# Performance work log

Hardware: AMD Instinct MI355X
Metric: run time of the kernel (lower is better)

## Reference

```python
import jax, jax.numpy as jnp
import numpy as np

N, E, F = 50000, 400000, 128
H0, C0 = 1, 128   # layer 0: heads=1, out=128 (concat=False -> mean over heads)
H1, C1 = 4, 64    # layer 1: heads=4, out=64
EPS_BN = 1e-5
NEG_SLOPE = 0.2


def setup_inputs() -> dict:
    key = jax.random.key(0)
    ks = jax.random.split(key, 12)

    def w(k, shape, fan_in):
        return jax.random.normal(k, shape, jnp.float32) / np.float32(np.sqrt(fan_in))

    return {
        "emb": jax.random.normal(ks[0], (N, F), jnp.float32),
        "edge_weight": jax.random.uniform(ks[1], (E,), jnp.float32),
        # GATv2Conv layer 0 params (lin_l, lin_r, lin_edge, att, out bias)
        "Wl0": w(ks[2], (F, H0 * C0), F), "bl0": jnp.zeros((H0 * C0,), jnp.float32),
        "Wr0": w(ks[3], (F, H0 * C0), F), "br0": jnp.zeros((H0 * C0,), jnp.float32),
        "We0": w(ks[4], (1, H0 * C0), 1), "att0": w(ks[5], (H0, C0), C0),
        "b0": jnp.zeros((C0,), jnp.float32),
        "g0": jnp.ones((C0,), jnp.float32), "be0": jnp.zeros((C0,), jnp.float32),
        # GATv2Conv layer 1 params
        "Wl1": w(ks[6], (C0, H1 * C1), C0), "bl1": jnp.zeros((H1 * C1,), jnp.float32),
        "Wr1": w(ks[7], (C0, H1 * C1), C0), "br1": jnp.zeros((H1 * C1,), jnp.float32),
        "We1": w(ks[8], (1, H1 * C1), 1), "att1": w(ks[9], (H1, C1), C1),
        "b1": jnp.zeros((C1,), jnp.float32),
        "g1": jnp.ones((C1,), jnp.float32), "be1": jnp.zeros((C1,), jnp.float32),
        "edge_index": jax.random.randint(ks[10], (2, E), 0, N, jnp.int32),
    }


def gatv2(x, src, dst, ea, Wl, bl, Wr, br, We, att, b, H, C):
    """PyG GATv2Conv, edge_dim=1, concat=False (mean over heads), eval dropout."""
    n = x.shape[0]
    xl = (x @ Wl + bl).reshape(n, H, C)
    xr = (x @ Wr + br).reshape(n, H, C)
    ef = (ea[:, None] @ We).reshape(-1, H, C)           # [Et,H,C] edge embedding
    m = jax.nn.leaky_relu(xl[src] + xr[dst] + ef, NEG_SLOPE)  # [Et,H,C]
    alpha = jnp.einsum('ehc,hc->eh', m, att)            # attention logits
    amax = jax.ops.segment_max(alpha, dst, num_segments=n)
    ex = jnp.exp(alpha - amax[dst])
    den = jax.ops.segment_sum(ex, dst, num_segments=n)
    a = ex / (den[dst] + 1e-16)                          # segment softmax (PyG eps)
    out = jax.ops.segment_sum(a[:, :, None] * xl[src], dst, num_segments=n)
    return out.mean(axis=1) + b                          # concat=False -> head mean


def batchnorm(x, g, be):
    mu = x.mean(0)
    v = x.var(0)  # biased variance, as torch BN uses for normalization
    return g * (x - mu) * jax.lax.rsqrt(v + EPS_BN) + be


def _forward(emb, edge_weight, Wl0, bl0, Wr0, br0, We0, att0, b0, g0, be0,
             Wl1, bl1, Wr1, br1, We1, att1, b1, g1, be1, edge_index):
    loop = jnp.arange(N, dtype=edge_index.dtype)
    src = jnp.concatenate([edge_index[0], loop])
    dst = jnp.concatenate([edge_index[1], loop])
    # add_self_loops with fill_value='mean' for edge_attr
    ea = jnp.concatenate([edge_weight, jnp.full((N,), edge_weight.mean(), edge_weight.dtype)])
    # NOTE: zip(layer_stack, batchnorm_stack) truncates -> only first 2 of 3 GAT
    # layers execute, each followed by BN + ELU (+ identity dropout, p=0).
    h = gatv2(emb, src, dst, ea, Wl0, bl0, Wr0, br0, We0, att0, b0, H0, C0)
    h = jax.nn.elu(batchnorm(h, g0, be0))
    h = gatv2(h, src, dst, ea, Wl1, bl1, Wr1, br1, We1, att1, b1, H1, C1)
    h = jax.nn.elu(batchnorm(h, g1, be1))
    return h


def reference(emb, edge_weight, Wl0, bl0, Wr0, br0, We0, att0, b0, g0, be0,
              Wl1, bl1, Wr1, br1, We1, att1, b1, g1, be1, edge_index):
    return _forward(emb, edge_weight, Wl0, bl0, Wr0, br0, We0, att0, b0, g0, be0,
                    Wl1, bl1, Wr1, br1, We1, att1, b1, g1, be1, edge_index)
```

## Files before the change

### kernel.cpp

```cpp
#include <hip/hip_runtime.h>
#include <cstdint>
#include <cstddef>
#include <type_traits>

using f32x4 = __attribute__((ext_vector_type(4))) float;
using s16x8 = __attribute__((ext_vector_type(8))) short;

__device__ __forceinline__ ushort f2bf(float x) {
    uint32_t u = __builtin_bit_cast(uint32_t, x);
    u += 0x7fffu + ((u >> 16) & 1u);
    return (ushort)(u >> 16);
}
__device__ __forceinline__ float bflo(uint32_t u) { return __builtin_bit_cast(float, u << 16); }
__device__ __forceinline__ float bfhi(uint32_t u) { return __builtin_bit_cast(float, u & 0xffff0000u); }

__device__ __forceinline__ void dec8(uint4 g, float* x) {
    x[0] = bflo(g.x); x[1] = bfhi(g.x); x[2] = bflo(g.y); x[3] = bfhi(g.y);
    x[4] = bflo(g.z); x[5] = bfhi(g.z); x[6] = bflo(g.w); x[7] = bfhi(g.w);
}

#define GLOAD_LDS16(g, l)                                                                  \
    __builtin_amdgcn_global_load_lds((const __attribute__((address_space(1))) void*)(g),  \
                                     (__attribute__((address_space(3))) void*)(l), 16, 0, 0)

__global__ __launch_bounds__(256) void degree_ew_wt(const int* __restrict__ ei,
                                                    const float* __restrict__ ew,
                                                    int* __restrict__ deg,
                                                    float* __restrict__ partials,
                                                    int E, int N, int NBE,
                                                    const float* __restrict__ Wl0,
                                                    const float* __restrict__ Wr0,
                                                    ushort* __restrict__ WT0,
                                                    const float* __restrict__ Wl1,
                                                    const float* __restrict__ Wr1,
                                                    ushort* __restrict__ WT1) {
    __shared__ float red[256];
    int bid = blockIdx.x;
    int t = threadIdx.x;
    if (bid < NBE) {
        int e = bid * 256 + t;
        float s = (e < E) ? ew[e] : 0.f;
        red[t] = s; __syncthreads();
        for (int o = 128; o; o >>= 1) { if (t < o) red[t] += red[t + o]; __syncthreads(); }
        if (t == 0) partials[bid] = red[0];
        if (e < E + N) {
            int d = (e < E) ? ei[E + e] : (e - E);
            atomicAdd(&deg[d], 1);
        }
        return;
    }
    int j = (bid - NBE) * 256 + t;
    if (j < 128 * 256) {
        int k = j >> 8, c = j & 255;
        float v = (c < 128) ? Wl0[k * 128 + c] : Wr0[k * 128 + (c - 128)];
        WT0[(size_t)c * 128 + k] = f2bf(v);
        return;
    }
    j -= 128 * 256;
    if (j < 128 * 512) {
        int k = j >> 9, c = j & 511;
        float v = (c < 256) ? Wl1[k * 256 + c] : Wr1[k * 256 + (c - 256)];
        WT1[(size_t)c * 128 + k] = f2bf(v);
    }
}

__global__ void scan_partial(const int* __restrict__ deg, int n, int* __restrict__ bsum) {
    __shared__ int lds[256];
    int t = threadIdx.x;
    int base = blockIdx.x * 1024 + t * 4;
    int s = 0;
#pragma unroll
    for (int j = 0; j < 4; ++j) if (base + j < n) s += deg[base + j];
    lds[t] = s; __syncthreads();
    for (int o = 128; o; o >>= 1) { if (t < o) lds[t] += lds[t + o]; __syncthreads(); }
    if (t == 0) bsum[blockIdx.x] = lds[0];
}

__global__ void scan_block(const int* __restrict__ bsum, int nb, int* __restrict__ boff,
                           int* __restrict__ row_start, int n, int total,
                           const float* __restrict__ partials, int nbp, int E,
                           float* __restrict__ stats) {
    __shared__ int lds[256];
    __shared__ float fred[256];
    int t = threadIdx.x;
    int v = (t < nb) ? bsum[t] : 0;
    lds[t] = v; __syncthreads();
    for (int o = 1; o < 256; o <<= 1) {
        int y = (t >= o) ? lds[t - o] : 0;
        __syncthreads();
        lds[t] += y;
        __syncthreads();
    }
    if (t < nb) boff[t] = lds[t] - v;
    if (t == 0) row_start[n] = total;
    stats[t] = 0.f; stats[256 + t] = 0.f;
    float fs = 0.f;
    for (int j = t; j < nbp; j += 256) fs += partials[j];
    fred[t] = fs; __syncthreads();
    for (int o = 128; o; o >>= 1) { if (t < o) fred[t] += fred[t + o]; __syncthreads(); }
    if (t == 0) stats[0] = fred[0] / (float)E;
}

__global__ void scan_final(const int* __restrict__ deg, int n, const int* __restrict__ boff,
                           int* __restrict__ row_start, int* __restrict__ cursor) {
    __shared__ int lds[256];
    int t = threadIdx.x;
    int base = blockIdx.x * 1024 + t * 4;
    int d[4], loc[4], s = 0;
#pragma unroll
    for (int j = 0; j < 4; ++j) d[j] = (base + j < n) ? deg[base + j] : 0;
#pragma unroll
    for (int j = 0; j < 4; ++j) { loc[j] = s; s += d[j]; }
    lds[t] = s; __syncthreads();
    for (int o = 1; o < 256; o <<= 1) {
        int y = (t >= o) ? lds[t - o] : 0;
        __syncthreads();
        lds[t] += y;
        __syncthreads();
    }
    int texcl = lds[t] - s + boff[blockIdx.x];
#pragma unroll
    for (int j = 0; j < 4; ++j)
        if (base + j < n) { row_start[base + j] = texcl + loc[j]; cursor[base + j] = 0; }
}

__global__ void scatter_kernel(const int* __restrict__ ei, const float* __restrict__ ew,
                               const float* __restrict__ ew_mean, const int* __restrict__ row_start,
                               int* __restrict__ cursor, int2* __restrict__ csr,
                               int E, int N) {
    int e = blockIdx.x * blockDim.x + threadIdx.x;
    if (e >= E + N) return;
    int s, d; float w;
    if (e < E) { s = ei[e]; d = ei[E + e]; w = ew[e]; }
    else       { s = d = e - E;            w = ew_mean[0]; }
    int pos = row_start[d] + atomicAdd(&cursor[d], 1);
    csr[pos] = make_int2(s, __builtin_bit_cast(int, w));
}

template <int MODE>
__global__ __launch_bounds__(512) void mfma_linear3(const void* __restrict__ Xv,
                                                    const ushort* __restrict__ WT,
                                                    const float* __restrict__ bnsums,
                                                    const float* __restrict__ gamma,
                                                    const float* __restrict__ beta,
                                                    const float* __restrict__ bl,
                                                    const float* __restrict__ br,
                                                    ushort* __restrict__ xl,
                                                    ushort* __restrict__ xr,
                                                    int n, int HALF) {
    constexpr int LW = (MODE == 1) ? 2 : 1;
    __shared__ ushort sB[128 * 128];
    __shared__ ushort sA[128 * 128];
    const int tid = threadIdx.x;
    const int c0 = blockIdx.x * 128;
    const int ntiles = (n + 127) >> 7;

    {
        const ushort* src = WT + (size_t)c0 * 128;
#pragma unroll
        for (int it = 0; it < 4; ++it) {
            int f = tid + it * 512;
            int row = f >> 4, ch = f & 15;
            const ushort* g = src + (size_t)row * 128 + ((ch ^ (row & 7)) << 3);
            ushort* lp = sB + (((size_t)it * 512 + (tid & ~63)) << 3);
            GLOAD_LDS16(g, lp);
        }
    }

    const int myc = (tid & 15) * 8;
    const int row0 = tid >> 4;
    const int swc = (tid & 15) ^ (row0 & 7);
    float Af[8], Bf[8];
    if constexpr (MODE == 2) {
        float invn = 1.f / (float)n;
#pragma unroll
        for (int j = 0; j < 8; ++j) {
            float mu = bnsums[myc + j] * invn;
            float var = bnsums[128 + myc + j] * invn - mu * mu;
            float rs = rsqrtf(var + 1e-5f);
            Af[j] = gamma[myc + j] * rs;
            Bf[j] = beta[myc + j] - mu * Af[j];
        }
    }

    uint4 rA[4][LW];
    auto loadA = [&](int rt) {
        int r0 = rt << 7;
#pragma unroll
        for (int it = 0; it < 4; ++it) {
            int gr = r0 + row0 + it * 32; gr = gr < n ? gr : n - 1;
            if constexpr (MODE == 1) {
                const float* src = (const float*)Xv + (size_t)gr * 128 + myc;
                rA[it][0] = *(const uint4*)src;
                rA[it][1] = *(const uint4*)(src + 4);
            } else {
                rA[it][0] = *(const uint4*)((const ushort*)Xv + (size_t)gr * 128 + myc);
            }
        }
    };
    auto writeA = [&]() {
#pragma unroll
        for (int it = 0; it < 4; ++it) {
            uint4 o;
            if constexpr (MODE == 0) {
                o = rA[it][0];
            } else if constexpr (MODE == 1) {
                float x[8] = {
                    __builtin_bit_cast(float, rA[it][0].x), __builtin_bit_cast(float, rA[it][0].y),
                    __builtin_bit_cast(float, rA[it][0].z), __builtin_bit_cast(float, rA[it][0].w),
                    __builtin_bit_cast(float, rA[it][1].x), __builtin_bit_cast(float, rA[it][1].y),
                    __builtin_bit_cast(float, rA[it][1].z), __builtin_bit_cast(float, rA[it][1].w)};
                ushort h[8];
#pragma unroll
                for (int j = 0; j < 8; ++j) h[j] = f2bf(x[j]);
                o.x = h[0] | ((uint32_t)h[1] << 16); o.y = h[2] | ((uint32_t)h[3] << 16);
                o.z = h[4] | ((uint32_t)h[5] << 16); o.w = h[6] | ((uint32_t)h[7] << 16);
            } else {
                float x[8]; dec8(rA[it][0], x);
                ushort h[8];
#pragma unroll
                for (int j = 0; j < 8; ++j) {
                    float v = fmaf(x[j], Af[j], Bf[j]);
                    v = v > 0.f ? v : __expf(v) - 1.f;
                    h[j] = f2bf(v);
                }
                o.x = h[0] | ((uint32_t)h[1] << 16); o.y = h[2] | ((uint32_t)h[3] << 16);
                o.z = h[4] | ((uint32_t)h[5] << 16); o.w = h[6] | ((uint32_t)h[7] << 16);
            }
            *(uint4*)&sA[(row0 + it * 32) * 128 + swc * 8] = o;
        }
    };

    const int w = tid >> 6, l = tid & 63, lr = l & 15, lg = l >> 4;
    const bool left = c0 < HALF;
    const float* bias = left ? bl : br;
    ushort* dst = left ? xl : xr;
    const int cb = left ? c0 : c0 - HALF;
    float bv[8];
#pragma unroll
    for (int tn = 0; tn < 8; ++tn) bv[tn] = bias[cb + tn * 16 + lr];
    const int arow = w * 16 + lr;

    int rt = blockIdx.y;
    if (rt >= ntiles) return;
    loadA(rt);
    writeA();
    __syncthreads();

    while (true) {
        int nx = rt + gridDim.y;
        if (nx < ntiles) loadA(nx);

        f32x4 acc[8] = {};
#pragma unroll
        for (int kk = 0; kk < 4; ++kk) {
            int ach = (kk * 4 + lg) ^ (arow & 7);
            s16x8 a = *(const s16x8*)&sA[arow * 128 + (ach << 3)];
#pragma unroll
            for (int tn = 0; tn < 8; ++tn) {
                int brow = tn * 16 + lr;
                int bch = (kk * 4 + lg) ^ (brow & 7);
                s16x8 b = *(const s16x8*)&sB[brow * 128 + (bch << 3)];
                acc[tn] = __builtin_amdgcn_mfma_f32_16x16x32_bf16(a, b, acc[tn], 0, 0, 0);
            }
        }
        int rbase = (rt << 7) + w * 16 + lg * 4;
#pragma unroll
        for (int tn = 0; tn < 8; ++tn) {
            int colh = cb + tn * 16 + lr;
#pragma unroll
            for (int r = 0; r < 4; ++r) {
                int row = rbase + r;
                if (row < n) dst[(size_t)row * HALF + colh] = f2bf(acc[tn][r] + bv[tn]);
            }
        }
        if (nx >= ntiles) break;
        __syncthreads();
        writeA();
        __syncthreads();
        rt = nx;
    }
}

template <int H, int C, int LPN>
__global__ __launch_bounds__(256, 6) void gat_agg(const ushort* __restrict__ xl,
                                                  const ushort* __restrict__ xr,
                                                  const int* __restrict__ row_start,
                                                  const int2* __restrict__ csr,
                                                  const float* __restrict__ We,
                                                  const float* __restrict__ att,
                                                  const float* __restrict__ bias,
                                                  ushort* __restrict__ out, int n) {
    constexpr int HC = H * C;
    constexpr int VPL = HC / LPN;
    constexpr int REDW = LPN / H;
    constexpr int NPW = 64 / LPN;
    static_assert(VPL == 8, "");

    const int wid = threadIdx.x >> 6;
    const int lane = threadIdx.x & 63;
    const int sl = lane & (LPN - 1);
    const int sub = lane / LPN;
    const int v = (blockIdx.x * 4 + wid) * NPW + sub;
    const bool valid = v < n;
    const int vv = valid ? v : n - 1;

    const int base = sl * VPL;
    const int e0 = row_start[vv];
    const int e1 = row_start[vv + 1];
    const ushort* xlb = xl + base;

    auto LD = [&](int ee, uint4& g, float& w) {
        ee = ee < e1 - 1 ? ee : e1 - 1;
        int2 sw = csr[ee];
        w = __builtin_bit_cast(float, sw.y);
        g = *(const uint4*)&xlb[(size_t)sw.x * HC];
    };

    uint4 gF; float wF;
    LD(e0, gF, wF);
    uint4 gA, gB; float wA, wB;
    LD(e0 + 1, gA, wA);
    LD(e0 + 2, gB, wB);

    float xrv[8], wE[8], attv[8];
    dec8(*(const uint4*)&xr[(size_t)vv * HC + base], xrv);
#pragma unroll
    for (int j = 0; j < 8; j += 4) {
        float4 a = *(const float4*)&We[base + j];
        wE[j] = a.x; wE[j + 1] = a.y; wE[j + 2] = a.z; wE[j + 3] = a.w;
        float4 b = *(const float4*)&att[base + j];
        attv[j] = b.x; attv[j + 1] = b.y; attv[j + 2] = b.z; attv[j + 3] = b.w;
    }

    float m, den, acc[8];
    {
        float xf[8];
        dec8(gF, xf);
        float t1 = 0.f, t2 = 0.f;
#pragma unroll
        for (int j = 0; j < 8; ++j) {
            float u = xf[j] + fmaf(wF, wE[j], xrv[j]);
            t1 = fmaf(u, attv[j], t1);
            t2 = fmaf(__builtin_fabsf(u), attv[j], t2);
        }
        float p = fmaf(0.6f, t1, 0.4f * t2);
#pragma unroll
        for (int o = REDW >> 1; o; o >>= 1) p += __shfl_xor(p, o, 64);
        m = p; den = 1.f;
#pragma unroll
        for (int j = 0; j < 8; ++j) acc[j] = xf[j];
    }

    int e = e0 + 1;
    while (e + 1 < e1) {
        uint4 g0 = gA, g1 = gB; float w0 = wA, w1 = wB;
        LD(e + 2, gA, wA);
        LD(e + 3, gB, wB);
        float xf0[8], xf1[8];
        dec8(g0, xf0); dec8(g1, xf1);
        float t10 = 0.f, t20 = 0.f, t11 = 0.f, t21 = 0.f;
#pragma unroll
        for (int j = 0; j < 8; ++j) {
            float u0 = xf0[j] + fmaf(w0, wE[j], xrv[j]);
            float u1 = xf1[j] + fmaf(w1, wE[j], xrv[j]);
            t10 = fmaf(u0, attv[j], t10);
            t20 = fmaf(__builtin_fabsf(u0), attv[j], t20);
            t11 = fmaf(u1, attv[j], t11);
            t21 = fmaf(__builtin_fabsf(u1), attv[j], t21);
        }
        float p0 = fmaf(0.6f, t10, 0.4f * t20);
        float p1 = fmaf(0.6f, t11, 0.4f * t21);
#pragma unroll
        for (int o = REDW >> 1; o; o >>= 1) {
            p0 += __shfl_xor(p0, o, 64);
            p1 += __shfl_xor(p1, o, 64);
        }
        float pm = fmaxf(p0, p1);
        if (__builtin_expect(pm - m > 8.f, 0)) {
            float r = __expf(m - pm);
            den *= r;
#pragma unroll
            for (int j = 0; j < 8; ++j) acc[j] *= r;
            m = pm;
        }
        float pe0 = __expf(p0 - m);
        float pe1 = __expf(p1 - m);
        den += pe0 + pe1;
#pragma unroll
        for (int j = 0; j < 8; ++j)
            acc[j] = fmaf(pe1, xf1[j], fmaf(pe0, xf0[j], acc[j]));
        e += 2;
    }
    if (e < e1) {
        float xf[8];
        dec8(gA, xf);
        float t1 = 0.f, t2 = 0.f;
#pragma unroll
        for (int j = 0; j < 8; ++j) {
            float u = xf[j] + fmaf(wA, wE[j], xrv[j]);
            t1 = fmaf(u, attv[j], t1);
            t2 = fmaf(__builtin_fabsf(u), attv[j], t2);
        }
        float p = fmaf(0.6f, t1, 0.4f * t2);
#pragma unroll
        for (int o = REDW >> 1; o; o >>= 1) p += __shfl_xor(p, o, 64);
        float dd = p - m;
        if (__builtin_expect(dd > 8.f, 0)) {
            float r = __expf(-dd);
            den = fmaf(den, r, 1.f);
#pragma unroll
            for (int j = 0; j < 8; ++j) acc[j] = fmaf(acc[j], r, xf[j]);
            m = p;
        } else {
            float pe = __expf(dd);
            den += pe;
#pragma unroll
            for (int j = 0; j < 8; ++j) acc[j] = fmaf(pe, xf[j], acc[j]);
        }
    }

    float inv = 1.f / den;
#pragma unroll
    for (int j = 0; j < 8; ++j) acc[j] *= inv;

    if constexpr (H > 1) {
#pragma unroll
        for (int o = REDW; o < LPN; o <<= 1)
#pragma unroll
            for (int j = 0; j < 8; ++j) acc[j] += __shfl_xor(acc[j], o, 64);
#pragma unroll
        for (int j = 0; j < 8; ++j) acc[j] *= (1.f / (float)H);
    }

    if (valid && sl < C / VPL) {
        float bv[8];
#pragma unroll
        for (int j = 0; j < 8; j += 4) {
            float4 b = *(const float4*)&bias[sl * VPL + j];
            bv[j] = b.x; bv[j + 1] = b.y; bv[j + 2] = b.z; bv[j + 3] = b.w;
        }
        uint4 o;
        o.x = (uint32_t)f2bf(acc[0] + bv[0]) | ((uint32_t)f2bf(acc[1] + bv[1]) << 16);
        o.y = (uint32_t)f2bf(acc[2] + bv[2]) | ((uint32_t)f2bf(acc[3] + bv[3]) << 16);
        o.z = (uint32_t)f2bf(acc[4] + bv[4]) | ((uint32_t)f2bf(acc[5] + bv[5]) << 16);
        o.w = (uint32_t)f2bf(acc[6] + bv[6]) | ((uint32_t)f2bf(acc[7] + bv[7]) << 16);
        *(uint4*)&out[(size_t)v * C + sl * VPL] = o;
    }
}

template <int C>
__global__ __launch_bounds__(256) void bn_stats_bf16(const ushort* __restrict__ x, int n,
                                                     float* __restrict__ sums) {
    constexpr int C2 = C / 2;
    constexpr int RPB = 256 / C2;
    __shared__ float red[256];
    int t = threadIdx.x;
    int c2 = t % C2, rs = t / C2;
    float s0 = 0.f, s1 = 0.f, q0 = 0.f, q1 = 0.f;
    for (int row = blockIdx.x * RPB + rs; row < n; row += gridDim.x * RPB) {
        uint32_t u = *(const uint32_t*)&x[(size_t)row * C + c2 * 2];
        float a = bflo(u), b = bfhi(u);
        s0 += a; q0 += a * a; s1 += b; q1 += b * b;
    }
    float vals[4] = {s0, s1, q0, q1};
    float outv[4];
#pragma unroll
    for (int k = 0; k < 4; ++k) {
        red[t] = vals[k]; __syncthreads();
        if (rs == 0) {
            float s = red[c2];
#pragma unroll
            for (int r = 1; r < RPB; ++r) s += red[c2 + r * C2];
            outv[k] = s;
        }
        __syncthreads();
    }
    if (rs == 0) {
        atomicAdd(&sums[c2 * 2],     outv[0]);
        atomicAdd(&sums[c2 * 2 + 1], outv[1]);
        atomicAdd(&sums[C + c2 * 2],     outv[2]);
        atomicAdd(&sums[C + c2 * 2 + 1], outv[3]);
    }
}

template <int C>
__global__ __launch_bounds__(256) void bn_apply_elu_f32(const ushort* __restrict__ x, int n,
                                                        const float* __restrict__ g,
                                                        const float* __restrict__ be,
                                                        const float* __restrict__ sums,
                                                        float* __restrict__ outf) {
    int total = n * C / 8;
    float invn = 1.f / (float)n;
    for (int i = blockIdx.x * blockDim.x + threadIdx.x; i < total; i += gridDim.x * blockDim.x) {
        uint4 u = ((const uint4*)x)[i];
        int c0 = (i * 8) & (C - 1);
        float r[8] = {bflo(u.x), bfhi(u.x), bflo(u.y), bfhi(u.y),
                      bflo(u.z), bfhi(u.z), bflo(u.w), bfhi(u.w)};
#pragma unroll
        for (int j = 0; j < 8; ++j) {
            int c = c0 + j;
            float mu = sums[c] * invn;
            float var = sums[C + c] * invn - mu * mu;
            float t = g[c] * (r[j] - mu) * rsqrtf(var + 1e-5f) + be[c];
            r[j] = t > 0.f ? t : expm1f(t);
        }
        ((float4*)outf)[i * 2]     = make_float4(r[0], r[1], r[2], r[3]);
        ((float4*)outf)[i * 2 + 1] = make_float4(r[4], r[5], r[6], r[7]);
    }
}

extern "C" void kernel_launch(void* const* d_in, const int* in_sizes, int n_in,
                              void* d_out, int out_size, void* d_ws, size_t ws_size,
                              hipStream_t stream) {
    const float* emb = (const float*)d_in[0];
    const float* ew  = (const float*)d_in[1];
    const float* Wl0 = (const float*)d_in[2];
    const float* bl0 = (const float*)d_in[3];
    const float* Wr0 = (const float*)d_in[4];
    const float* br0 = (const float*)d_in[5];
    const float* We0 = (const float*)d_in[6];
    const float* att0 = (const float*)d_in[7];
    const float* b0  = (const float*)d_in[8];
    const float* g0  = (const float*)d_in[9];
    const float* be0 = (const float*)d_in[10];
    const float* Wl1 = (const float*)d_in[11];
    const float* bl1 = (const float*)d_in[12];
    const float* Wr1 = (const float*)d_in[13];
    const float* br1 = (const float*)d_in[14];
    const float* We1 = (const float*)d_in[15];
    const float* att1 = (const float*)d_in[16];
    const float* b1  = (const float*)d_in[17];
    const float* g1  = (const float*)d_in[18];
    const float* be1 = (const float*)d_in[19];
    const int* ei    = (const int*)d_in[20];

    const int N = in_sizes[0] / 128;
    const int E = in_sizes[1];
    const int Et = E + N;
    float* out = (float*)d_out;

    char* w = (char*)d_ws;
    size_t off = 0;
    auto alloc = [&](size_t bytes) {
        void* p = w + off;
        off = (off + bytes + 255) & ~(size_t)255;
        return p;
    };
    ushort* xlb    = (ushort*)alloc((size_t)N * 256 * 2);
    ushort* xrb    = (ushort*)alloc((size_t)N * 256 * 2);
    ushort* h0b16  = (ushort*)alloc((size_t)N * 128 * 2);
    ushort* out16  = (ushort*)alloc((size_t)N * 64 * 2);
    ushort* WT0    = (ushort*)alloc((size_t)256 * 128 * 2);
    ushort* WT1    = (ushort*)alloc((size_t)512 * 128 * 2);
    int*   deg     = (int*)alloc((size_t)2 * N * 4);
    int*   cursor  = deg + N;
    int*   row_st  = (int*)alloc((size_t)(N + 1) * 4);
    int2*  csr     = (int2*)alloc((size_t)(Et + 8) * 8);
    int*   bsum    = (int*)alloc(256 * 4);
    int*   boff    = (int*)alloc(256 * 4);
    float* partials= (float*)alloc(2048 * 4);
    float* stats   = (float*)alloc(512 * 4);
    float* ew_mean = stats;
    float* bn0     = stats + 64;
    float* bn1     = stats + 64 + 256;
    (void)ws_size; (void)n_in; (void)out_size;

    hipMemsetAsync(deg, 0, (size_t)N * 4, stream);

    const int NBE = (Et + 255) / 256;
    const int WTB = (128 * 256 + 128 * 512) / 256;
    degree_ew_wt<<<NBE + WTB, 256, 0, stream>>>(ei, ew, deg, partials, E, N, NBE,
                                                Wl0, Wr0, WT0, Wl1, Wr1, WT1);
    const int NB1 = (N + 1023) / 1024;
    scan_partial<<<NB1, 256, 0, stream>>>(deg, N, bsum);
    scan_block<<<1, 256, 0, stream>>>(bsum, NB1, boff, row_st, N, Et, partials, NBE, E, stats);
    scan_final<<<NB1, 256, 0, stream>>>(deg, N, boff, row_st, cursor);
    scatter_kernel<<<NBE, 256, 0, stream>>>(ei, ew, ew_mean, row_st, cursor, csr, E, N);

    const int ntiles = (N + 127) / 128;
    const int GR = ntiles < 256 ? ntiles : 256;

    mfma_linear3<1><<<dim3(2, GR), 512, 0, stream>>>(emb, WT0, nullptr, nullptr, nullptr,
                                                     bl0, br0, xlb, xrb, N, 128);
    gat_agg<1, 128, 16><<<(N + 15) / 16, 256, 0, stream>>>(xlb, xrb, row_st, csr,
                                                           We0, att0, b0, h0b16, N);
    bn_stats_bf16<128><<<256, 256, 0, stream>>>(h0b16, N, bn0);

    mfma_linear3<2><<<dim3(4, GR), 512, 0, stream>>>(h0b16, WT1, bn0, g0, be0,
                                                     bl1, br1, xlb, xrb, N, 256);
    gat_agg<4, 64, 32><<<(N + 7) / 8, 256, 0, stream>>>(xlb, xrb, row_st, csr,
                                                        We1, att1, b1, out16, N);
    bn_stats_bf16<64><<<256, 256, 0, stream>>>(out16, N, bn1);
    bn_apply_elu_f32<64><<<1024, 256, 0, stream>>>(out16, N, g1, be1, bn1, out);
}
```

Measured before the change: 240.6 us.

## Bucket nodes by degree so GAT aggregation waves process similar-degree nodes

Builds a degree histogram (capped at 63) during the scan kernels and counting-sorts node ids into a permutation array. Both gat_agg launches then map each wave slot to a node through this permutation, so nodes sharing a wave have similar edge counts and lanes idle less. The cost is extra atomics in the scan kernels, one more indirection per node, and output writes that are no longer contiguous across waves. Bucket order within a block is nondeterministic, but each node's result is unchanged.

```diff
diff --git a/kernel.cpp b/kernel.cpp
--- a/kernel.cpp
+++ b/kernel.cpp
@@ -64,22 +64,34 @@
     }
 }
 
-__global__ void scan_partial(const int* __restrict__ deg, int n, int* __restrict__ bsum) {
+__global__ void scan_partial(const int* __restrict__ deg, int n, int* __restrict__ bsum,
+                             int* __restrict__ bcnt) {
     __shared__ int lds[256];
+    __shared__ int hist[64];
     int t = threadIdx.x;
     int base = blockIdx.x * 1024 + t * 4;
-    int s = 0;
-#pragma unroll
-    for (int j = 0; j < 4; ++j) if (base + j < n) s += deg[base + j];
-    lds[t] = s; __syncthreads();
+    int dd[4], s = 0;
+#pragma unroll
+    for (int j = 0; j < 4; ++j) {
+        dd[j] = (base + j < n) ? deg[base + j] : -1;
+        if (dd[j] >= 0) s += dd[j];
+    }
+    lds[t] = s;
+    if (t < 64) hist[t] = 0;
+    __syncthreads();
+#pragma unroll
+    for (int j = 0; j < 4; ++j)
+        if (dd[j] >= 0) atomicAdd(&hist[dd[j] < 63 ? dd[j] : 63], 1);
     for (int o = 128; o; o >>= 1) { if (t < o) lds[t] += lds[t + o]; __syncthreads(); }
     if (t == 0) bsum[blockIdx.x] = lds[0];
+    if (t < 64 && hist[t]) atomicAdd(&bcnt[t], hist[t]);
 }
 
 __global__ void scan_block(const int* __restrict__ bsum, int nb, int* __restrict__ boff,
                            int* __restrict__ row_start, int n, int total,
                            const float* __restrict__ partials, int nbp, int E,
-                           float* __restrict__ stats) {
+                           float* __restrict__ stats,
+                           const int* __restrict__ bcnt, int* __restrict__ bcursor) {
     __shared__ int lds[256];
     __shared__ float fred[256];
     int t = threadIdx.x;
@@ -99,10 +111,21 @@
     fred[t] = fs; __syncthreads();
     for (int o = 128; o; o >>= 1) { if (t < o) fred[t] += fred[t + o]; __syncthreads(); }
     if (t == 0) stats[0] = fred[0] / (float)E;
+    __syncthreads();
+    int bvv = (t < 64) ? bcnt[t] : 0;
+    lds[t] = bvv; __syncthreads();
+    for (int o = 1; o < 64; o <<= 1) {
+        int y = (t >= o && t < 64) ? lds[t - o] : 0;
+        __syncthreads();
+        if (t < 64) lds[t] += y;
+        __syncthreads();
+    }
+    if (t < 64) bcursor[t] = lds[t] - bvv;
 }
 
 __global__ void scan_final(const int* __restrict__ deg, int n, const int* __restrict__ boff,
-                           int* __restrict__ row_start, int* __restrict__ cursor) {
+                           int* __restrict__ row_start, int* __restrict__ cursor,
+                           int* __restrict__ bcursor, int* __restrict__ perm) {
     __shared__ int lds[256];
     int t = threadIdx.x;
     int base = blockIdx.x * 1024 + t * 4;
@@ -122,6 +145,24 @@
 #pragma unroll
     for (int j = 0; j < 4; ++j)
         if (base + j < n) { row_start[base + j] = texcl + loc[j]; cursor[base + j] = 0; }
+    __syncthreads();
+    if (t < 64) { lds[t] = 0; lds[128 + t] = 0; }
+    __syncthreads();
+    int bk[4];
+#pragma unroll
+    for (int j = 0; j < 4; ++j) {
+        bk[j] = d[j] < 63 ? d[j] : 63;
+        if (base + j < n) atomicAdd(&lds[bk[j]], 1);
+    }
+    __syncthreads();
+    if (t < 64 && lds[t] > 0) lds[64 + t] = atomicAdd(&bcursor[t], lds[t]);
+    __syncthreads();
+#pragma unroll
+    for (int j = 0; j < 4; ++j)
+        if (base + j < n) {
+            int pos = lds[64 + bk[j]] + atomicAdd(&lds[128 + bk[j]], 1);
+            perm[pos] = base + j;
+        }
 }
 
 __global__ void scatter_kernel(const int* __restrict__ ei, const float* __restrict__ ew,
@@ -287,6 +328,7 @@
                                                   const ushort* __restrict__ xr,
                                                   const int* __restrict__ row_start,
                                                   const int2* __restrict__ csr,
+                                                  const int* __restrict__ perm,
                                                   const float* __restrict__ We,
                                                   const float* __restrict__ att,
                                                   const float* __restrict__ bias,
@@ -301,9 +343,9 @@
     const int lane = threadIdx.x & 63;
     const int sl = lane & (LPN - 1);
     const int sub = lane / LPN;
-    const int v = (blockIdx.x * 4 + wid) * NPW + sub;
-    const bool valid = v < n;
-    const int vv = valid ? v : n - 1;
+    const int slot = (blockIdx.x * 4 + wid) * NPW + sub;
+    const bool valid = slot < n;
+    const int vv = perm[valid ? slot : n - 1];
 
     const int base = sl * VPL;
     const int e0 = row_start[vv];
@@ -445,7 +487,7 @@
         o.y = (uint32_t)f2bf(acc[2] + bv[2]) | ((uint32_t)f2bf(acc[3] + bv[3]) << 16);
         o.z = (uint32_t)f2bf(acc[4] + bv[4]) | ((uint32_t)f2bf(acc[5] + bv[5]) << 16);
         o.w = (uint32_t)f2bf(acc[6] + bv[6]) | ((uint32_t)f2bf(acc[7] + bv[7]) << 16);
-        *(uint4*)&out[(size_t)v * C + sl * VPL] = o;
+        *(uint4*)&out[(size_t)vv * C + sl * VPL] = o;
     }
 }
 
@@ -553,8 +595,11 @@
     ushort* out16  = (ushort*)alloc((size_t)N * 64 * 2);
     ushort* WT0    = (ushort*)alloc((size_t)256 * 128 * 2);
     ushort* WT1    = (ushort*)alloc((size_t)512 * 128 * 2);
-    int*   deg     = (int*)alloc((size_t)2 * N * 4);
-    int*   cursor  = deg + N;
+    int*   deg     = (int*)alloc(((size_t)2 * N + 128) * 4);
+    int*   bcnt    = deg + N;
+    int*   cursor  = deg + N + 64;
+    int*   bcursor = deg + 2 * N + 64;
+    int*   perm    = (int*)alloc((size_t)N * 4);
     int*   row_st  = (int*)alloc((size_t)(N + 1) * 4);
     int2*  csr     = (int2*)alloc((size_t)(Et + 8) * 8);
     int*   bsum    = (int*)alloc(256 * 4);
@@ -566,16 +611,17 @@
     float* bn1     = stats + 64 + 256;
     (void)ws_size; (void)n_in; (void)out_size;
 
-    hipMemsetAsync(deg, 0, (size_t)N * 4, stream);
+    hipMemsetAsync(deg, 0, ((size_t)N + 64) * 4, stream);
 
     const int NBE = (Et + 255) / 256;
     const int WTB = (128 * 256 + 128 * 512) / 256;
     degree_ew_wt<<<NBE + WTB, 256, 0, stream>>>(ei, ew, deg, partials, E, N, NBE,
                                                 Wl0, Wr0, WT0, Wl1, Wr1, WT1);
     const int NB1 = (N + 1023) / 1024;
-    scan_partial<<<NB1, 256, 0, stream>>>(deg, N, bsum);
-    scan_block<<<1, 256, 0, stream>>>(bsum, NB1, boff, row_st, N, Et, partials, NBE, E, stats);
-    scan_final<<<NB1, 256, 0, stream>>>(deg, N, boff, row_st, cursor);
+    scan_partial<<<NB1, 256, 0, stream>>>(deg, N, bsum, bcnt);
+    scan_block<<<1, 256, 0, stream>>>(bsum, NB1, boff, row_st, N, Et, partials, NBE, E,
+                                      stats, bcnt, bcursor);
+    scan_final<<<NB1, 256, 0, stream>>>(deg, N, boff, row_st, cursor, bcursor, perm);
     scatter_kernel<<<NBE, 256, 0, stream>>>(ei, ew, ew_mean, row_st, cursor, csr, E, N);
 
     const int ntiles = (N + 127) / 128;
@@ -583,13 +629,13 @@
 
     mfma_linear3<1><<<dim3(2, GR), 512, 0, stream>>>(emb, WT0, nullptr, nullptr, nullptr,
                                                      bl0, br0, xlb, xrb, N, 128);
-    gat_agg<1, 128, 16><<<(N + 15) / 16, 256, 0, stream>>>(xlb, xrb, row_st, csr,
+    gat_agg<1, 128, 16><<<(N + 15) / 16, 256, 0, stream>>>(xlb, xrb, row_st, csr, perm,
                                                            We0, att0, b0, h0b16, N);
     bn_stats_bf16<128><<<256, 256, 0, stream>>>(h0b16, N, bn0);
 
     mfma_linear3<2><<<dim3(4, GR), 512, 0, stream>>>(h0b16, WT1, bn0, g0, be0,
                                                      bl1, br1, xlb, xrb, N, 256);
-    gat_agg<4, 64, 32><<<(N + 7) / 8, 256, 0, stream>>>(xlb, xrb, row_st, csr,
+    gat_agg<4, 64, 32><<<(N + 7) / 8, 256, 0, stream>>>(xlb, xrb, row_st, csr, perm,
                                                         We1, att1, b1, out16, N);
     bn_stats_bf16<64><<<256, 256, 0, stream>>>(out16, N, bn1);
     bn_apply_elu_f32<64><<<1024, 256, 0, stream>>>(out16, N, g1, be1, bn1, out);
```

New measurement: 242.9 us. Within noise of the previous version (+1.0%).
